# Optimization experiments

Measured on AMD Instinct MI355X. Metric: run time of the kernel, lower is better.

Reference implementation:

```python
import jax, jax.numpy as jnp
import numpy as np

THRESHOLD = 10.0

def _sig(x):
    # sigmoid((x - 0.5) * threshold)
    return jax.nn.sigmoid((x - 0.5) * THRESHOLD)

def _sobel1d(x):
    # Conv1d kernel [-1, 0, 1], padding=1, per-channel (weights are diagonal across channels)
    p = jnp.pad(x, ((0, 0), (0, 0), (1, 1)))
    return p[..., 2:] - p[..., :-2]

def _structs(x_sig, direction):
    # x_sig: [B, C, H, W]
    p = jnp.pad(x_sig, ((0, 0), (0, 0), (1, 1), (1, 1)))
    if direction == 'x':
        # sobelx kernel: w[0,0]=-1, w[2,0]=1 -> out[i,j] = t[i+1,j-1] - t[i-1,j-1]
        bound = _sig(jnp.abs(p[..., 2:, :-2] - p[..., :-2, :-2]))
        s = bound.sum(-2)  # [B, C, W]
    else:
        # sobely kernel: w[0,0]=-1, w[0,2]=1 -> out[i,j] = t[i-1,j+1] - t[i-1,j-1]
        bound = _sig(jnp.abs(p[..., :-2, 2:] - p[..., :-2, :-2]))
        s = bound.sum(-1)  # [B, C, H]
    return jnp.abs(_sobel1d(s)).sum(-1) / 4.0  # [B, C]

def setup_inputs() -> dict:
    key = jax.random.key(0)
    k1, k2 = jax.random.split(key)
    B, C, H, W = 16, 4, 512, 512
    inp = jax.random.uniform(k1, (B, C, H, W), dtype=jnp.float32)
    tgt = jax.random.uniform(k2, (B, C, H, W), dtype=jnp.float32)
    weight = jnp.ones((1, C), dtype=jnp.float32)
    return {"input": inp, "target": tgt, "weight": weight}

def reference(input, target, weight):
    input_sigmoid = _sig(input)
    target_sigmoid = _sig(target)
    input_structs_x = _structs(input_sigmoid, 'x') * weight
    input_structs_y = _structs(input_sigmoid, 'y') * weight
    target_structs_x = _structs(target_sigmoid, 'x') * weight
    target_structs_y = _structs(target_sigmoid, 'y') * weight
    loss = (jnp.abs(input_structs_x - target_structs_x)
            + jnp.abs(input_structs_y - target_structs_y)) / 2.0
    return jnp.mean(loss)
```

## Files before the change

### kernel.cpp

```cpp
#include <hip/hip_runtime.h>

#define WW 512
#define HH 512
#define NPLANES 64
#define NCH 4
#define NSTRIP 8

__device__ __forceinline__ float expu(float x) {
    return __builtin_amdgcn_exp2f(__builtin_fmaf(x, -14.4269504089f, 7.2134752044f));
}
__device__ __forceinline__ float sigf(float x) {
    return __builtin_amdgcn_rcpf(1.0f + expu(x));
}
__device__ __forceinline__ float sum4sig(float p0, float p1, float p2, float p3) {
    float q01 = p0 * p1, q23 = p2 * p3;
    float inv = __builtin_amdgcn_rcpf(q01 * q23);
    return __builtin_fmaf(p0 + p1, q23, (p2 + p3) * q01) * inv;
}
__device__ __forceinline__ void inv4(float p0, float p1, float p2, float p3,
                                     float& r0, float& r1, float& r2, float& r3) {
    float q01 = p0 * p1, q23 = p2 * p3;
    float inv = __builtin_amdgcn_rcpf(q01 * q23);
    float i01 = q23 * inv, i23 = q01 * inv;
    r0 = p1 * i01; r1 = p0 * i01;
    r2 = p3 * i23; r3 = p2 * i23;
}

__global__ __launch_bounds__(256, 4)
void k_stage1(const float* __restrict__ inp, const float* __restrict__ tgt,
              float* __restrict__ colpart, float* __restrict__ rowsum8,
              float* __restrict__ out) {
    const int bid    = blockIdx.x;
    const int tensor = bid >> 9;
    const int plane  = (bid >> 3) & 63;
    const int s      = bid & 7;
    const int tid    = threadIdx.x;
    const int wave   = tid >> 6;
    const int lane   = tid & 63;

    if (bid == 0 && tid == 0) out[0] = 0.0f;

    const float* __restrict__ base =
        (tensor == 0 ? inp : tgt) + (size_t)plane * (HH * WW);
    const int r0    = s * 64 + wave * 16;
    const int r1    = r0 + 16;
    const int cbase = lane * 8;

    float prev[8], cur[8], cacc[8];
    #pragma unroll
    for (int k = 0; k < 8; ++k) cacc[k] = 0.0f;

    if (r0 == 0) {
        #pragma unroll
        for (int k = 0; k < 8; ++k) prev[k] = 0.0f;
    } else {
        const float4* p4 = reinterpret_cast<const float4*>(base + (size_t)(r0 - 1) * WW + cbase);
        float4 a = p4[0], b = p4[1];
        prev[0]=sigf(a.x); prev[1]=sigf(a.y); prev[2]=sigf(a.z); prev[3]=sigf(a.w);
        prev[4]=sigf(b.x); prev[5]=sigf(b.y); prev[6]=sigf(b.z); prev[7]=sigf(b.w);
    }
    {
        const float4* p4 = reinterpret_cast<const float4*>(base + (size_t)r0 * WW + cbase);
        float4 a = p4[0], b = p4[1];
        cur[0]=sigf(a.x); cur[1]=sigf(a.y); cur[2]=sigf(a.z); cur[3]=sigf(a.w);
        cur[4]=sigf(b.x); cur[5]=sigf(b.y); cur[6]=sigf(b.z); cur[7]=sigf(b.w);
    }

    float* __restrict__ rs_out =
        rowsum8 + ((size_t)tensor * NPLANES + plane) * (HH * 8);

    const float* rowp = base + (size_t)(r0 + 1) * WW + cbase;

    for (int r = r0; r < r1; ++r, rowp += WW) {
        float4 a, b;
        if (r + 1 < HH) {
            const float4* p4 = reinterpret_cast<const float4*>(rowp);
            a = p4[0]; b = p4[1];
        } else {
            a = make_float4(0.f,0.f,0.f,0.f); b = a;
        }

        float lv = __shfl_up(cur[7], 1);
        if (lane == 0)  lv = 0.0f;
        float rv = __shfl_down(cur[0], 1);
        if (lane == 63) rv = 0.0f;

        float h0 = 1.0f + expu(fabsf(cur[1] - lv));
        float h1 = 1.0f + expu(fabsf(cur[2] - cur[0]));
        float h2 = 1.0f + expu(fabsf(cur[3] - cur[1]));
        float h3 = 1.0f + expu(fabsf(cur[4] - cur[2]));
        float h4 = 1.0f + expu(fabsf(cur[5] - cur[3]));
        float h5 = 1.0f + expu(fabsf(cur[6] - cur[4]));
        float h6 = 1.0f + expu(fabsf(cur[7] - cur[5]));
        float h7 = 1.0f + expu(fabsf(rv     - cur[6]));
        float hp = sum4sig(h0, h1, h2, h3) + sum4sig(h4, h5, h6, h7);

        hp += __shfl_xor(hp, 8);
        hp += __shfl_xor(hp, 16);
        hp += __shfl_xor(hp, 32);
        if (lane < 8) rs_out[(size_t)r * 8 + lane] = hp;

        float nxt[8];
        if (r + 1 < HH) {
            float p0 = 1.0f + expu(a.x), p1 = 1.0f + expu(a.y);
            float p2 = 1.0f + expu(a.z), p3 = 1.0f + expu(a.w);
            float p4_ = 1.0f + expu(b.x), p5 = 1.0f + expu(b.y);
            float p6 = 1.0f + expu(b.z), p7 = 1.0f + expu(b.w);
            inv4(p0, p1, p2, p3, nxt[0], nxt[1], nxt[2], nxt[3]);
            inv4(p4_, p5, p6, p7, nxt[4], nxt[5], nxt[6], nxt[7]);
        } else {
            #pragma unroll
            for (int k = 0; k < 8; ++k) nxt[k] = 0.0f;
        }

        {
            float v0 = 1.0f + expu(fabsf(nxt[0] - prev[0]));
            float v1 = 1.0f + expu(fabsf(nxt[1] - prev[1]));
            float v2 = 1.0f + expu(fabsf(nxt[2] - prev[2]));
            float v3 = 1.0f + expu(fabsf(nxt[3] - prev[3]));
            float v4 = 1.0f + expu(fabsf(nxt[4] - prev[4]));
            float v5 = 1.0f + expu(fabsf(nxt[5] - prev[5]));
            float v6 = 1.0f + expu(fabsf(nxt[6] - prev[6]));
            float v7 = 1.0f + expu(fabsf(nxt[7] - prev[7]));
            float s0, s1, s2, s3, s4, s5, s6, s7;
            inv4(v0, v1, v2, v3, s0, s1, s2, s3);
            inv4(v4, v5, v6, v7, s4, s5, s6, s7);
            cacc[0] += s0; cacc[1] += s1; cacc[2] += s2; cacc[3] += s3;
            cacc[4] += s4; cacc[5] += s5; cacc[6] += s6; cacc[7] += s7;
        }

        #pragma unroll
        for (int k = 0; k < 8; ++k) { prev[k] = cur[k]; cur[k] = nxt[k]; }
    }

    __shared__ float cl[4][WW];
    #pragma unroll
    for (int k = 0; k < 8; ++k) cl[wave][cbase + k] = cacc[k];
    __syncthreads();

    float* __restrict__ cp_out =
        colpart + (((size_t)tensor * NPLANES + plane) * NSTRIP + s) * WW;
    for (int c = tid; c < WW; c += 256)
        cp_out[c] = cl[0][c] + cl[1][c] + cl[2][c] + cl[3][c];
}

__device__ __forceinline__ float Sval(const float* s, int j, float s0) {
    if (j < 0 || j >= 512) return 0.0f;
    if (j == 0) return s0;
    return s[j - 1];
}
__device__ __forceinline__ float term(const float* s, int j, float s0) {
    return fabsf(Sval(s, j + 1, s0) - Sval(s, j - 1, s0));
}

__global__ __launch_bounds__(256)
void k_stage2(const float* __restrict__ colpart, const float* __restrict__ rowsum8,
              const float* __restrict__ weight, float* __restrict__ out) {
    __shared__ float cI[WW], cT[WW], rI[WW], rT[WW];
    const int p   = blockIdx.x;
    const int tid = threadIdx.x;

    for (int c = tid; c < WW; c += 256) {
        const float* a = colpart + (((size_t)0 * NPLANES + p) * NSTRIP) * WW + c;
        const float* b = colpart + (((size_t)1 * NPLANES + p) * NSTRIP) * WW + c;
        float sa = 0.f, sb = 0.f;
        #pragma unroll
        for (int i = 0; i < NSTRIP; ++i) { sa += a[i * WW]; sb += b[i * WW]; }
        cI[c] = sa;
        cT[c] = sb;
        const float* ra = rowsum8 + ((size_t)0 * NPLANES + p) * (HH * 8) + (size_t)c * 8;
        const float* rb = rowsum8 + ((size_t)1 * NPLANES + p) * (HH * 8) + (size_t)c * 8;
        float sra = 0.f, srb = 0.f;
        #pragma unroll
        for (int i = 0; i < 8; ++i) { sra += ra[i]; srb += rb[i]; }
        rI[c] = sra;
        rT[c] = srb;
    }
    __syncthreads();

    const float s0 = 3.4267396732f;

    float sIx = 0.f, sTx = 0.f, sIy = 0.f, sTy = 0.f;
    for (int j = tid; j < WW; j += 256) {
        sIx += term(cI, j, s0);
        sTx += term(cT, j, s0);
        sIy += term(rI, j, s0);
        sTy += term(rT, j, s0);
    }
    #pragma unroll
    for (int off = 32; off >= 1; off >>= 1) {
        sIx += __shfl_xor(sIx, off);
        sTx += __shfl_xor(sTx, off);
        sIy += __shfl_xor(sIy, off);
        sTy += __shfl_xor(sTy, off);
    }
    __shared__ float red[4][4];
    const int wave = tid >> 6, lane = tid & 63;
    if (lane == 0) {
        red[wave][0] = sIx; red[wave][1] = sTx;
        red[wave][2] = sIy; red[wave][3] = sTy;
    }
    __syncthreads();
    if (tid == 0) {
        float Ix = 0.f, Tx = 0.f, Iy = 0.f, Ty = 0.f;
        for (int w2 = 0; w2 < 4; ++w2) {
            Ix += red[w2][0]; Tx += red[w2][1];
            Iy += red[w2][2]; Ty += red[w2][3];
        }
        Ix *= 0.25f; Tx *= 0.25f; Iy *= 0.25f; Ty *= 0.25f;
        const float wgt = weight[p & (NCH - 1)];
        float loss = 0.5f * (fabsf((Ix - Tx) * wgt) + fabsf((Iy - Ty) * wgt));
        atomicAdd(out, loss * (1.0f / NPLANES));
    }
}

extern "C" void kernel_launch(void* const* d_in, const int* in_sizes, int n_in,
                              void* d_out, int out_size, void* d_ws, size_t ws_size,
                              hipStream_t stream) {
    const float* inp = (const float*)d_in[0];
    const float* tgt = (const float*)d_in[1];
    const float* wgt = (const float*)d_in[2];
    float* ws = (float*)d_ws;

    float* colpart = ws;
    float* rowsum8 = ws + 524288;

    k_stage1<<<1024, 256, 0, stream>>>(inp, tgt, colpart, rowsum8, (float*)d_out);
    k_stage2<<<64, 256, 0, stream>>>(colpart, rowsum8, wgt, (float*)d_out);
}
```

Baseline: 154.1 us.

## Prefetch next row one iteration ahead and split stage2 by direction

Stage1 now issues the global load for row r+2 while computing row r, software-pipelining the streaming loads so memory latency overlaps the transcendental math. Stage2 is split into 128 blocks, one per plane and direction, so the column and row reductions run in parallel across twice as many blocks. The cost is extra registers for the prefetched row and twice as many atomics on the output.

```diff
diff --git a/kernel.cpp b/kernel.cpp
--- a/kernel.cpp
+++ b/kernel.cpp
@@ -55,29 +55,35 @@
         for (int k = 0; k < 8; ++k) prev[k] = 0.0f;
     } else {
         const float4* p4 = reinterpret_cast<const float4*>(base + (size_t)(r0 - 1) * WW + cbase);
-        float4 a = p4[0], b = p4[1];
-        prev[0]=sigf(a.x); prev[1]=sigf(a.y); prev[2]=sigf(a.z); prev[3]=sigf(a.w);
-        prev[4]=sigf(b.x); prev[5]=sigf(b.y); prev[6]=sigf(b.z); prev[7]=sigf(b.w);
+        float4 a0 = p4[0], b0 = p4[1];
+        prev[0]=sigf(a0.x); prev[1]=sigf(a0.y); prev[2]=sigf(a0.z); prev[3]=sigf(a0.w);
+        prev[4]=sigf(b0.x); prev[5]=sigf(b0.y); prev[6]=sigf(b0.z); prev[7]=sigf(b0.w);
     }
     {
         const float4* p4 = reinterpret_cast<const float4*>(base + (size_t)r0 * WW + cbase);
-        float4 a = p4[0], b = p4[1];
-        cur[0]=sigf(a.x); cur[1]=sigf(a.y); cur[2]=sigf(a.z); cur[3]=sigf(a.w);
-        cur[4]=sigf(b.x); cur[5]=sigf(b.y); cur[6]=sigf(b.z); cur[7]=sigf(b.w);
+        float4 a0 = p4[0], b0 = p4[1];
+        cur[0]=sigf(a0.x); cur[1]=sigf(a0.y); cur[2]=sigf(a0.z); cur[3]=sigf(a0.w);
+        cur[4]=sigf(b0.x); cur[5]=sigf(b0.y); cur[6]=sigf(b0.z); cur[7]=sigf(b0.w);
+    }
+
+    float4 a, b;
+    {
+        const float4* p4 = reinterpret_cast<const float4*>(base + (size_t)(r0 + 1) * WW + cbase);
+        a = p4[0]; b = p4[1];
     }
 
     float* __restrict__ rs_out =
         rowsum8 + ((size_t)tensor * NPLANES + plane) * (HH * 8);
 
-    const float* rowp = base + (size_t)(r0 + 1) * WW + cbase;
-
-    for (int r = r0; r < r1; ++r, rowp += WW) {
-        float4 a, b;
-        if (r + 1 < HH) {
-            const float4* p4 = reinterpret_cast<const float4*>(rowp);
-            a = p4[0]; b = p4[1];
+    const float* rowp2 = base + (size_t)(r0 + 2) * WW + cbase;
+
+    for (int r = r0; r < r1; ++r, rowp2 += WW) {
+        float4 na, nb;
+        if (r + 2 < HH) {
+            const float4* p4 = reinterpret_cast<const float4*>(rowp2);
+            na = p4[0]; nb = p4[1];
         } else {
-            a = make_float4(0.f,0.f,0.f,0.f); b = a;
+            na = make_float4(0.f,0.f,0.f,0.f); nb = na;
         }
 
         float lv = __shfl_up(cur[7], 1);
@@ -131,6 +137,7 @@
 
         #pragma unroll
         for (int k = 0; k < 8; ++k) { prev[k] = cur[k]; cur[k] = nxt[k]; }
+        a = na; b = nb;
     }
 
     __shared__ float cl[4][WW];
@@ -156,60 +163,56 @@
 __global__ __launch_bounds__(256)
 void k_stage2(const float* __restrict__ colpart, const float* __restrict__ rowsum8,
               const float* __restrict__ weight, float* __restrict__ out) {
-    __shared__ float cI[WW], cT[WW], rI[WW], rT[WW];
-    const int p   = blockIdx.x;
+    __shared__ float sI[WW], sT[WW];
+    const int p   = blockIdx.x >> 1;
+    const int dir = blockIdx.x & 1;
     const int tid = threadIdx.x;
 
-    for (int c = tid; c < WW; c += 256) {
-        const float* a = colpart + (((size_t)0 * NPLANES + p) * NSTRIP) * WW + c;
-        const float* b = colpart + (((size_t)1 * NPLANES + p) * NSTRIP) * WW + c;
-        float sa = 0.f, sb = 0.f;
-        #pragma unroll
-        for (int i = 0; i < NSTRIP; ++i) { sa += a[i * WW]; sb += b[i * WW]; }
-        cI[c] = sa;
-        cT[c] = sb;
-        const float* ra = rowsum8 + ((size_t)0 * NPLANES + p) * (HH * 8) + (size_t)c * 8;
-        const float* rb = rowsum8 + ((size_t)1 * NPLANES + p) * (HH * 8) + (size_t)c * 8;
-        float sra = 0.f, srb = 0.f;
-        #pragma unroll
-        for (int i = 0; i < 8; ++i) { sra += ra[i]; srb += rb[i]; }
-        rI[c] = sra;
-        rT[c] = srb;
+    if (dir == 0) {
+        for (int c = tid; c < WW; c += 256) {
+            const float* a = colpart + (((size_t)0 * NPLANES + p) * NSTRIP) * WW + c;
+            const float* b = colpart + (((size_t)1 * NPLANES + p) * NSTRIP) * WW + c;
+            float sa = 0.f, sb = 0.f;
+            #pragma unroll
+            for (int i = 0; i < NSTRIP; ++i) { sa += a[i * WW]; sb += b[i * WW]; }
+            sI[c] = sa;
+            sT[c] = sb;
+        }
+    } else {
+        for (int c = tid; c < WW; c += 256) {
+            const float* ra = rowsum8 + ((size_t)0 * NPLANES + p) * (HH * 8) + (size_t)c * 8;
+            const float* rb = rowsum8 + ((size_t)1 * NPLANES + p) * (HH * 8) + (size_t)c * 8;
+            float sra = 0.f, srb = 0.f;
+            #pragma unroll
+            for (int i = 0; i < 8; ++i) { sra += ra[i]; srb += rb[i]; }
+            sI[c] = sra;
+            sT[c] = srb;
+        }
     }
     __syncthreads();
 
     const float s0 = 3.4267396732f;
 
-    float sIx = 0.f, sTx = 0.f, sIy = 0.f, sTy = 0.f;
+    float sumI = 0.f, sumT = 0.f;
     for (int j = tid; j < WW; j += 256) {
-        sIx += term(cI, j, s0);
-        sTx += term(cT, j, s0);
-        sIy += term(rI, j, s0);
-        sTy += term(rT, j, s0);
+        sumI += term(sI, j, s0);
+        sumT += term(sT, j, s0);
     }
     #pragma unroll
     for (int off = 32; off >= 1; off >>= 1) {
-        sIx += __shfl_xor(sIx, off);
-        sTx += __shfl_xor(sTx, off);
-        sIy += __shfl_xor(sIy, off);
-        sTy += __shfl_xor(sTy, off);
-    }
-    __shared__ float red[4][4];
+        sumI += __shfl_xor(sumI, off);
+        sumT += __shfl_xor(sumT, off);
+    }
+    __shared__ float red[4][2];
     const int wave = tid >> 6, lane = tid & 63;
-    if (lane == 0) {
-        red[wave][0] = sIx; red[wave][1] = sTx;
-        red[wave][2] = sIy; red[wave][3] = sTy;
-    }
+    if (lane == 0) { red[wave][0] = sumI; red[wave][1] = sumT; }
     __syncthreads();
     if (tid == 0) {
-        float Ix = 0.f, Tx = 0.f, Iy = 0.f, Ty = 0.f;
-        for (int w2 = 0; w2 < 4; ++w2) {
-            Ix += red[w2][0]; Tx += red[w2][1];
-            Iy += red[w2][2]; Ty += red[w2][3];
-        }
-        Ix *= 0.25f; Tx *= 0.25f; Iy *= 0.25f; Ty *= 0.25f;
+        float I = 0.f, T = 0.f;
+        for (int w2 = 0; w2 < 4; ++w2) { I += red[w2][0]; T += red[w2][1]; }
+        I *= 0.25f; T *= 0.25f;
         const float wgt = weight[p & (NCH - 1)];
-        float loss = 0.5f * (fabsf((Ix - Tx) * wgt) + fabsf((Iy - Ty) * wgt));
+        float loss = 0.5f * fabsf((I - T) * wgt);
         atomicAdd(out, loss * (1.0f / NPLANES));
     }
 }
@@ -226,5 +229,5 @@
     float* rowsum8 = ws + 524288;
 
     k_stage1<<<1024, 256, 0, stream>>>(inp, tgt, colpart, rowsum8, (float*)d_out);
-    k_stage2<<<64, 256, 0, stream>>>(colpart, rowsum8, wgt, (float*)d_out);
-}
+    k_stage2<<<128, 256, 0, stream>>>(colpart, rowsum8, wgt, (float*)d_out);
+}
```

After: 155.9 us. About the same (+1.2%).
